# Kernel tuning notes

Hardware: AMD Instinct MI355X
Metric: run time of the kernel (lower is better)

## Reference

```python
import jax, jax.numpy as jnp
import numpy as np


def setup_inputs() -> dict:
    key = jax.random.key(0)
    ks = jax.random.split(key, 12)
    N, E, D_IN, D_H, R, B, G, C, D_E = 50000, 600000, 128, 128, 8, 4, 64, 16, 16
    x = jax.random.normal(ks[0], (N, D_IN), dtype=jnp.float32)
    edge_index = jax.random.randint(ks[1], (2, E), 0, N, dtype=jnp.int64)
    edge_type = jax.random.randint(ks[2], (E,), 0, R, dtype=jnp.int64)
    edge_attr = jax.random.normal(ks[3], (E, D_E), dtype=jnp.float32)
    batch = jnp.sort(jax.random.randint(ks[4], (N,), 0, G, dtype=jnp.int64))
    # RGCNConv basis-decomposition params + root + bias
    basis = jax.random.normal(ks[5], (B, D_IN, D_H), dtype=jnp.float32) / np.sqrt(D_IN)
    comp = jax.random.normal(ks[6], (R, B), dtype=jnp.float32) / np.sqrt(B)
    root = jax.random.normal(ks[7], (D_IN, D_H), dtype=jnp.float32) / np.sqrt(D_IN)
    bias = jnp.zeros((D_H,), dtype=jnp.float32)
    fc_w = jax.random.normal(ks[8], (D_H, C), dtype=jnp.float32) / np.sqrt(D_H)
    fc_b = jnp.zeros((C,), dtype=jnp.float32)
    return {"x": x, "edge_index": edge_index, "edge_type": edge_type,
            "edge_attr": edge_attr, "batch": batch, "num_graphs": 64,
            "basis": basis, "comp": comp, "root": root, "bias": bias,
            "fc_w": fc_w, "fc_b": fc_b}


def reference(x, edge_index, edge_type, edge_attr, batch, num_graphs,
              basis, comp, root, bias, fc_w, fc_b):
    N = x.shape[0]
    R = comp.shape[0]
    src, dst = edge_index[0], edge_index[1]
    # relation weights from basis decomposition: [R, in, out]
    W = jnp.einsum('rb,bio->rio', comp, basis)
    x_src = x[src]  # gather source features [E, in]
    agg = jnp.zeros((N, W.shape[2]), dtype=x.dtype)
    # per-relation mean aggregation (PyG RGCNConv default), summed over relations
    for r in range(R):
        mask = (edge_type == r).astype(x.dtype)  # [E]
        msg = (x_src @ W[r]) * mask[:, None]     # [E, out]
        summed = jax.ops.segment_sum(msg, dst, num_segments=N)
        cnt = jax.ops.segment_sum(mask, dst, num_segments=N)
        agg = agg + summed / jnp.maximum(cnt, 1.0)[:, None]
    h = jax.nn.relu(x @ root + bias + agg)       # [N, hidden]
    # global mean pool over graphs
    pooled_sum = jax.ops.segment_sum(h, batch, num_segments=num_graphs)
    gcnt = jax.ops.segment_sum(jnp.ones((N,), dtype=x.dtype), batch, num_segments=num_graphs)
    pooled = pooled_sum / jnp.maximum(gcnt, 1.0)[:, None]  # [G, hidden]
    return pooled @ fc_w + fc_b                  # [G, num_classes]
```

## Files before the change

kernel.cpp:

```cpp
#include <hip/hip_runtime.h>

static inline int ceil_div(int a, int b){ return (a+b-1)/b; }
static inline size_t align_up(size_t x, size_t a){ return (x + a - 1) / a * a; }

typedef __bf16 bf16x8 __attribute__((ext_vector_type(8)));
typedef float  f32x4  __attribute__((ext_vector_type(4)));

static __device__ inline unsigned short f2bf(float f){
    unsigned int u = __float_as_uint(f);
    unsigned int lsb = (u >> 16) & 1u;
    u += 0x7FFFu + lsb;
    return (unsigned short)(u >> 16);
}
static __device__ inline float bf2f(unsigned short b){
    return __uint_as_float(((unsigned int)b) << 16);
}
static __device__ inline unsigned int packbf(float a, float b){
    return (unsigned int)f2bf(a) | ((unsigned int)f2bf(b) << 16);
}

static __device__ inline void gload_lds16(const void* g, void* l) {
    __builtin_amdgcn_global_load_lds(
        (const __attribute__((address_space(1))) unsigned int*)g,
        (__attribute__((address_space(3))) unsigned int*)l, 16, 0, 0);
}

__global__ void compute_Bt_kernel(const float* __restrict__ comp, const float* __restrict__ basis,
                                  const float* __restrict__ root, unsigned short* __restrict__ Bt,
                                  int B) {
    int idx = blockIdx.x*blockDim.x + threadIdx.x;
    if (idx >= 128*1152) return;
    int o = idx / 1152, kk = idx - o*1152;
    float val;
    if (kk < 1024) {
        int r = kk >> 7, i = kk & 127;
        val = 0.f;
        for (int b = 0; b < B; ++b)
            val += comp[r*B+b] * basis[((size_t)b*128 + i)*128 + o];
    } else {
        val = root[(size_t)(kk-1024)*128 + o];
    }
    Bt[idx] = f2bf(val);
}

__global__ void count_kernel(const int* __restrict__ dst, const int* __restrict__ et,
                             int* __restrict__ cnt, int E, int R) {
    int e = blockIdx.x*blockDim.x + threadIdx.x;
    if (e >= E) return;
    atomicAdd(&cnt[(size_t)dst[e]*R + et[e]], 1);
}

__global__ __launch_bounds__(256)
void scan_block_kernel(const int* __restrict__ in, int* __restrict__ out,
                       int* __restrict__ bsums, int n) {
    __shared__ int tsum[256];
    int t = threadIdx.x;
    int idx0 = blockIdx.x*1024 + t*4;
    int v0 = (idx0+0 < n) ? in[idx0+0] : 0;
    int v1 = (idx0+1 < n) ? in[idx0+1] : 0;
    int v2 = (idx0+2 < n) ? in[idx0+2] : 0;
    int v3 = (idx0+3 < n) ? in[idx0+3] : 0;
    int s = v0+v1+v2+v3;
    tsum[t] = s; __syncthreads();
    for (int off = 1; off < 256; off <<= 1) {
        int x = (t >= off) ? tsum[t-off] : 0;
        __syncthreads();
        tsum[t] += x;
        __syncthreads();
    }
    int run = tsum[t] - s;
    if (idx0+0 < n) out[idx0+0] = run; run += v0;
    if (idx0+1 < n) out[idx0+1] = run; run += v1;
    if (idx0+2 < n) out[idx0+2] = run; run += v2;
    if (idx0+3 < n) out[idx0+3] = run;
    if (bsums && t == 255) bsums[blockIdx.x] = tsum[255];
}

__global__ void scan_add_kernel(int* __restrict__ out, const int* __restrict__ bs,
                                int n, int total) {
    int i = blockIdx.x*blockDim.x + threadIdx.x;
    if (i < n) out[i] += bs[i >> 10];
    if (i == 0) out[n] = total;
}

__global__ void fill_kernel(const int* __restrict__ src, const int* __restrict__ dst,
                            const int* __restrict__ et, int* __restrict__ offsets,
                            int* __restrict__ slot_src, int E, int R) {
    int e = blockIdx.x*blockDim.x + threadIdx.x;
    if (e >= E) return;
    if (e < 4) slot_src[E + e] = 0;
    int bin = dst[e]*R + et[e];
    int slot = atomicAdd(&offsets[bin], 1);
    slot_src[slot] = src[e];
}

__global__ __launch_bounds__(256)
void xb_kernel(const float* __restrict__ x, unsigned int* __restrict__ Xb2, int N) {
    int t = blockIdx.x*blockDim.x + threadIdx.x;
    int n = t >> 6;
    if (n >= N) return;
    int l = t & 63;
    float2 v = reinterpret_cast<const float2*>(x + (size_t)n*128)[l];
    Xb2[(size_t)n*64 + l] = packbf(v.x, v.y);
}

__global__ __launch_bounds__(256)
void aggregate_kernel(const int* __restrict__ offsets, const int* __restrict__ slot_src,
                      const unsigned int* __restrict__ Xb2, unsigned int* __restrict__ Mc2,
                      int N) {
    int gw = (int)((blockIdx.x*blockDim.x + threadIdx.x) >> 6);
    int node = gw >> 2, part = gw & 3;
    if (node >= N) return;
    int l = threadIdx.x & 63;
    int base = node*8 + part*2;
    int lo   = (base == 0) ? 0 : offsets[base-1];
    int bmid = offsets[base];
    int hi   = offsets[base+1];

    float ax0=0.f, ay0=0.f, ax1=0.f, ay1=0.f;

#define ACC2(E_, U_) { \
    float vx_ = bf2f((unsigned short)((U_) & 0xFFFFu)); \
    float vy_ = bf2f((unsigned short)((U_) >> 16)); \
    if ((E_) < bmid) { ax0 += vx_; ay0 += vy_; } \
    else             { ax1 += vx_; ay1 += vy_; } }

    for (int e = lo; e < hi; e += 4) {
        int s0 = slot_src[e];
        int s1 = slot_src[e+1];
        int s2 = slot_src[e+2];
        int s3 = slot_src[e+3];
        unsigned int u0 = Xb2[(size_t)s0*64 + l];
        unsigned int u1 = Xb2[(size_t)s1*64 + l];
        unsigned int u2 = Xb2[(size_t)s2*64 + l];
        unsigned int u3 = Xb2[(size_t)s3*64 + l];
        if (e+1 >= hi) u1 = 0u;
        if (e+2 >= hi) u2 = 0u;
        if (e+3 >= hi) u3 = 0u;
        ACC2(e+0, u0) ACC2(e+1, u1) ACC2(e+2, u2) ACC2(e+3, u3)
    }
#undef ACC2

    unsigned int* Mrow = Mc2 + (size_t)node*512;
    float i0 = 1.f/fmaxf((float)(bmid-lo), 1.f);
    float i1 = 1.f/fmaxf((float)(hi-bmid), 1.f);
    __builtin_nontemporal_store(packbf(ax0*i0, ay0*i0), &Mrow[(2*part+0)*64 + l]);
    __builtin_nontemporal_store(packbf(ax1*i1, ay1*i1), &Mrow[(2*part+1)*64 + l]);
}

__global__ __launch_bounds__(256)
void mfma_gemm_kernel(const unsigned short* __restrict__ Mc,
                      const unsigned short* __restrict__ Xb,
                      const unsigned short* __restrict__ Btc,
                      const float* __restrict__ bias,
                      unsigned short* __restrict__ h, int MBrows) {
    __shared__ char ldsA[64*128];
    __shared__ char ldsB[64*128];

    int tid  = threadIdx.x;
    int lane = tid & 63;
    int wid  = tid >> 6;
    int rg = wid & 1, cg = wid >> 1;
    int fr = lane & 15, kb = lane >> 4;

    int blk = blockIdx.x;
    int q = blk >> 4, rem = blk & 15, c = rem >> 3, m = rem & 7;
    int rb = q*8 + m;
    if (rb >= MBrows) return;
    long m0 = (long)rb * 64;
    int colbase = c * 64;

    int lrow8 = lane >> 3;
    int lcb   = (lane & 7) * 16;

    f32x4 acc[2][2];
    #pragma unroll
    for (int mf = 0; mf < 2; ++mf)
        #pragma unroll
        for (int nf = 0; nf < 2; ++nf) acc[mf][nf] = f32x4{0.f,0.f,0.f,0.f};

    const char* McB = (const char*)Mc;
    const char* XbB = (const char*)Xb;
    const char* BtB = (const char*)Btc;

    for (int t = 0; t < 18; ++t) {
        #pragma unroll
        for (int i = 0; i < 2; ++i) {
            int row = wid*16 + i*8 + lrow8;
            int sw  = lcb ^ ((row & 7) << 4);
            const char* g = (t < 16)
                ? McB + (size_t)(m0 + row)*2048 + t*128 + sw
                : XbB + (size_t)(m0 + row)*256 + (t-16)*128 + sw;
            gload_lds16(g, &ldsA[wid*2048 + i*1024 + lane*16]);
        }
        #pragma unroll
        for (int i = 0; i < 2; ++i) {
            int col = wid*16 + i*8 + lrow8;
            int sw  = lcb ^ ((col & 7) << 4);
            const char* g = BtB + (size_t)(colbase + col)*2304 + t*128 + sw;
            gload_lds16(g, &ldsB[wid*2048 + i*1024 + lane*16]);
        }
        __syncthreads();

        bf16x8 af[2][2], bfr[2][2];
        #pragma unroll
        for (int mf = 0; mf < 2; ++mf) {
            int row = rg*32 + mf*16 + fr;
            #pragma unroll
            for (int kk = 0; kk < 2; ++kk) {
                int byte = row*128 + ((kk*64 + kb*16) ^ ((row & 7) << 4));
                af[mf][kk] = *reinterpret_cast<const bf16x8*>(&ldsA[byte]);
            }
        }
        #pragma unroll
        for (int nf = 0; nf < 2; ++nf) {
            int col = cg*32 + nf*16 + fr;
            #pragma unroll
            for (int kk = 0; kk < 2; ++kk) {
                int byte = col*128 + ((kk*64 + kb*16) ^ ((col & 7) << 4));
                bfr[nf][kk] = *reinterpret_cast<const bf16x8*>(&ldsB[byte]);
            }
        }
        #pragma unroll
        for (int kk = 0; kk < 2; ++kk)
            #pragma unroll
            for (int mf = 0; mf < 2; ++mf)
                #pragma unroll
                for (int nf = 0; nf < 2; ++nf)
                    acc[mf][nf] = __builtin_amdgcn_mfma_f32_16x16x32_bf16(
                        af[mf][kk], bfr[nf][kk], acc[mf][nf], 0, 0, 0);
        __syncthreads();
    }

    float bb[2];
    #pragma unroll
    for (int nf = 0; nf < 2; ++nf) bb[nf] = bias[colbase + cg*32 + nf*16 + fr];

    #pragma unroll
    for (int mf = 0; mf < 2; ++mf)
        #pragma unroll
        for (int q2 = 0; q2 < 4; ++q2) {
            long r = m0 + rg*32 + mf*16 + kb*4 + q2;
            unsigned short* hr = h + (size_t)r*128 + colbase + cg*32;
            #pragma unroll
            for (int nf = 0; nf < 2; ++nf)
                hr[nf*16 + fr] = f2bf(fmaxf(acc[mf][nf][q2] + bb[nf], 0.f));
        }
}

__global__ __launch_bounds__(256)
void pool_kernel(const unsigned int* __restrict__ h2, const int* __restrict__ batch,
                 float* __restrict__ psum, int N) {
    int g = blockIdx.x;
    int t = threadIdx.x;
    int lo = 0, hi = N;
    while (lo < hi) { int mid = (lo+hi) >> 1; if (batch[mid] < g) lo = mid+1; else hi = mid; }
    int s0 = lo;
    hi = N;
    while (lo < hi) { int mid = (lo+hi) >> 1; if (batch[mid] < g+1) lo = mid+1; else hi = mid; }
    int s1 = lo;
    int len = s1 - s0;
    int chunk = blockIdx.y, NC = gridDim.y;
    int a = s0 + (int)((long long)len * chunk / NC);
    int b = s0 + (int)((long long)len * (chunk+1) / NC);

    int d2 = t & 63;
    float ax = 0.f, ay = 0.f;
    for (int row = a + (t >> 6); row < b; row += 4) {
        unsigned int u = h2[(size_t)row*64 + d2];
        ax += bf2f((unsigned short)(u & 0xFFFFu));
        ay += bf2f((unsigned short)(u >> 16));
    }
    atomicAdd(&psum[(size_t)g*128 + 2*d2    ], ax);
    atomicAdd(&psum[(size_t)g*128 + 2*d2 + 1], ay);
}

__global__ void fc_kernel(const float* __restrict__ psum, const int* __restrict__ batch,
                          const float* __restrict__ fw, const float* __restrict__ fb,
                          float* __restrict__ out, int N, int G, int C) {
    int idx = blockIdx.x*blockDim.x + threadIdx.x;
    if (idx >= G*C) return;
    int g = idx / C, cc = idx - g*C;
    int lo = 0, hi = N;
    while (lo < hi) { int mid = (lo+hi) >> 1; if (batch[mid] < g) lo = mid+1; else hi = mid; }
    int s0 = lo;
    hi = N;
    while (lo < hi) { int mid = (lo+hi) >> 1; if (batch[mid] < g+1) lo = mid+1; else hi = mid; }
    float inv = 1.f / fmaxf((float)(lo - s0), 1.f);
    float s = fb[cc];
    #pragma unroll 4
    for (int k = 0; k < 128; ++k)
        s += psum[(size_t)g*128 + k] * inv * fw[(size_t)k*C + cc];
    out[idx] = s;
}

extern "C" void kernel_launch(void* const* d_in, const int* in_sizes, int n_in,
                              void* d_out, int out_size, void* d_ws, size_t ws_size,
                              hipStream_t stream) {
    const float* x       = (const float*)d_in[0];
    const int*   eindex  = (const int*)  d_in[1];
    const int*   etype   = (const int*)  d_in[2];
    const int*   batch   = (const int*)  d_in[4];
    const float* basis   = (const float*)d_in[6];
    const float* comp    = (const float*)d_in[7];
    const float* root    = (const float*)d_in[8];
    const float* bias    = (const float*)d_in[9];
    const float* fc_w    = (const float*)d_in[10];
    const float* fc_b    = (const float*)d_in[11];

    int N  = in_sizes[4];
    int E  = in_sizes[2];
    int C  = in_sizes[11];
    int G  = out_size / C;
    int IO = in_sizes[8];
    int B  = in_sizes[6] / IO;
    int R  = in_sizes[7] / B;
    int NR = N * R;
    int MB = ceil_div(N, 64);
    int Mpad = MB * 64;
    int grid_gemm = ceil_div(MB, 8) * 16;

    const int* src = eindex;
    const int* dst = eindex + E;

    char* base = (char*)d_ws;
    size_t off = 0;
    auto alloc = [&](size_t bytes) -> char* {
        char* p = base + off;
        off = align_up(off + bytes, 256);
        return p;
    };
    unsigned short* Bt  = (unsigned short*)alloc(sizeof(unsigned short)*128*1152);
    int*   cnt      = (int*)  alloc(sizeof(int)*(size_t)NR);
    float* psum     = (float*)alloc(sizeof(float)*(size_t)G*128);
    int*   offsets  = (int*)  alloc(sizeof(int)*((size_t)NR+1));
    int*   bsums    = (int*)  alloc(sizeof(int)*1024);
    int*   slot_src = (int*)  alloc(sizeof(int)*((size_t)E+4));
    unsigned short* h  = (unsigned short*)alloc(sizeof(unsigned short)*(size_t)Mpad*128);
    unsigned short* Xb = (unsigned short*)alloc(sizeof(unsigned short)*(size_t)Mpad*128);
    unsigned short* Mc = (unsigned short*)alloc(sizeof(unsigned short)*(size_t)Mpad*1024);

    hipMemsetAsync(cnt, 0, (size_t)((char*)(psum + (size_t)G*128) - (char*)cnt), stream);
    compute_Bt_kernel<<<ceil_div(128*1152,256),256,0,stream>>>(comp, basis, root, Bt, B);
    count_kernel<<<ceil_div(E,256),256,0,stream>>>(dst, etype, cnt, E, R);

    int nb = ceil_div(NR, 1024);
    scan_block_kernel<<<nb,256,0,stream>>>(cnt, offsets, bsums, NR);
    scan_block_kernel<<<1,256,0,stream>>>(bsums, bsums, nullptr, nb);
    scan_add_kernel<<<ceil_div(NR,256),256,0,stream>>>(offsets, bsums, NR, E);

    fill_kernel<<<ceil_div(E,256),256,0,stream>>>(src, dst, etype, offsets, slot_src, E, R);

    xb_kernel<<<ceil_div(N*64,256),256,0,stream>>>(x, (unsigned int*)Xb, N);
    aggregate_kernel<<<ceil_div(N*4*64,256),256,0,stream>>>(offsets, slot_src,
                                                            (const unsigned int*)Xb,
                                                            (unsigned int*)Mc, N);

    mfma_gemm_kernel<<<grid_gemm,256,0,stream>>>(Mc, Xb, Bt, bias, h, MB);

    pool_kernel<<<dim3(G,8),256,0,stream>>>((const unsigned int*)h, batch, psum, N);
    fc_kernel<<<ceil_div(G*C,256),256,0,stream>>>(psum, batch, fc_w, fc_b,
                                                  (float*)d_out, N, G, C);
}
```

Measured before the change: 217.4 us.

## Widen GEMM tile to full output width with double-buffered LDS staging

The GEMM block now computes all 128 output columns for its 64 rows instead of splitting into two column halves. This halves re-reads of the large aggregated-message matrix. LDS tiles are double-buffered so the next k-slice load is issued before computing the current one. The fill kernel also stores pre-shifted row offsets so the aggregate gather skips a 64-bit multiply. The trade-off is more LDS and accumulator registers per block, with half as many blocks.

```diff
diff --git a/kernel.cpp b/kernel.cpp
--- a/kernel.cpp
+++ b/kernel.cpp
@@ -85,13 +85,13 @@
 
 __global__ void fill_kernel(const int* __restrict__ src, const int* __restrict__ dst,
                             const int* __restrict__ et, int* __restrict__ offsets,
-                            int* __restrict__ slot_src, int E, int R) {
+                            int* __restrict__ slot_off, int E, int R) {
     int e = blockIdx.x*blockDim.x + threadIdx.x;
     if (e >= E) return;
-    if (e < 4) slot_src[E + e] = 0;
+    if (e < 4) slot_off[E + e] = 0;
     int bin = dst[e]*R + et[e];
     int slot = atomicAdd(&offsets[bin], 1);
-    slot_src[slot] = src[e];
+    slot_off[slot] = src[e] << 6;
 }
 
 __global__ __launch_bounds__(256)
@@ -105,7 +105,7 @@
 }
 
 __global__ __launch_bounds__(256)
-void aggregate_kernel(const int* __restrict__ offsets, const int* __restrict__ slot_src,
+void aggregate_kernel(const int* __restrict__ offsets, const int* __restrict__ slot_off,
                       const unsigned int* __restrict__ Xb2, unsigned int* __restrict__ Mc2,
                       int N) {
     int gw = (int)((blockIdx.x*blockDim.x + threadIdx.x) >> 6);
@@ -126,14 +126,14 @@
     else             { ax1 += vx_; ay1 += vy_; } }
 
     for (int e = lo; e < hi; e += 4) {
-        int s0 = slot_src[e];
-        int s1 = slot_src[e+1];
-        int s2 = slot_src[e+2];
-        int s3 = slot_src[e+3];
-        unsigned int u0 = Xb2[(size_t)s0*64 + l];
-        unsigned int u1 = Xb2[(size_t)s1*64 + l];
-        unsigned int u2 = Xb2[(size_t)s2*64 + l];
-        unsigned int u3 = Xb2[(size_t)s3*64 + l];
+        int s0 = slot_off[e];
+        int s1 = slot_off[e+1];
+        int s2 = slot_off[e+2];
+        int s3 = slot_off[e+3];
+        unsigned int u0 = Xb2[(unsigned)(s0 + l)];
+        unsigned int u1 = Xb2[(unsigned)(s1 + l)];
+        unsigned int u2 = Xb2[(unsigned)(s2 + l)];
+        unsigned int u3 = Xb2[(unsigned)(s3 + l)];
         if (e+1 >= hi) u1 = 0u;
         if (e+2 >= hi) u2 = 0u;
         if (e+3 >= hi) u3 = 0u;
@@ -153,37 +153,31 @@
                       const unsigned short* __restrict__ Xb,
                       const unsigned short* __restrict__ Btc,
                       const float* __restrict__ bias,
-                      unsigned short* __restrict__ h, int MBrows) {
-    __shared__ char ldsA[64*128];
-    __shared__ char ldsB[64*128];
+                      unsigned short* __restrict__ h) {
+    __shared__ char ldsA[2][64*128];
+    __shared__ char ldsB[2][128*128];
 
     int tid  = threadIdx.x;
     int lane = tid & 63;
     int wid  = tid >> 6;
     int rg = wid & 1, cg = wid >> 1;
     int fr = lane & 15, kb = lane >> 4;
-
-    int blk = blockIdx.x;
-    int q = blk >> 4, rem = blk & 15, c = rem >> 3, m = rem & 7;
-    int rb = q*8 + m;
-    if (rb >= MBrows) return;
-    long m0 = (long)rb * 64;
-    int colbase = c * 64;
+    long m0 = (long)blockIdx.x * 64;
 
     int lrow8 = lane >> 3;
     int lcb   = (lane & 7) * 16;
-
-    f32x4 acc[2][2];
-    #pragma unroll
-    for (int mf = 0; mf < 2; ++mf)
-        #pragma unroll
-        for (int nf = 0; nf < 2; ++nf) acc[mf][nf] = f32x4{0.f,0.f,0.f,0.f};
 
     const char* McB = (const char*)Mc;
     const char* XbB = (const char*)Xb;
     const char* BtB = (const char*)Btc;
 
-    for (int t = 0; t < 18; ++t) {
+    f32x4 acc[2][4];
+    #pragma unroll
+    for (int mf = 0; mf < 2; ++mf)
+        #pragma unroll
+        for (int nf = 0; nf < 4; ++nf) acc[mf][nf] = f32x4{0.f,0.f,0.f,0.f};
+
+    auto stage = [&](int t, int buf) {
         #pragma unroll
         for (int i = 0; i < 2; ++i) {
             int row = wid*16 + i*8 + lrow8;
@@ -191,34 +185,41 @@
             const char* g = (t < 16)
                 ? McB + (size_t)(m0 + row)*2048 + t*128 + sw
                 : XbB + (size_t)(m0 + row)*256 + (t-16)*128 + sw;
-            gload_lds16(g, &ldsA[wid*2048 + i*1024 + lane*16]);
-        }
-        #pragma unroll
-        for (int i = 0; i < 2; ++i) {
-            int col = wid*16 + i*8 + lrow8;
+            gload_lds16(g, &ldsA[buf][wid*2048 + i*1024 + lane*16]);
+        }
+        #pragma unroll
+        for (int i = 0; i < 4; ++i) {
+            int col = wid*32 + i*8 + lrow8;
             int sw  = lcb ^ ((col & 7) << 4);
-            const char* g = BtB + (size_t)(colbase + col)*2304 + t*128 + sw;
-            gload_lds16(g, &ldsB[wid*2048 + i*1024 + lane*16]);
-        }
-        __syncthreads();
-
-        bf16x8 af[2][2], bfr[2][2];
+            const char* g = BtB + (size_t)col*2304 + t*128 + sw;
+            gload_lds16(g, &ldsB[buf][wid*4096 + i*1024 + lane*16]);
+        }
+    };
+
+    stage(0, 0);
+    __syncthreads();
+
+    for (int t = 0; t < 18; ++t) {
+        int cur = t & 1;
+        if (t + 1 < 18) stage(t + 1, cur ^ 1);
+
+        bf16x8 af[2][2], bfr[4][2];
         #pragma unroll
         for (int mf = 0; mf < 2; ++mf) {
             int row = rg*32 + mf*16 + fr;
             #pragma unroll
             for (int kk = 0; kk < 2; ++kk) {
                 int byte = row*128 + ((kk*64 + kb*16) ^ ((row & 7) << 4));
-                af[mf][kk] = *reinterpret_cast<const bf16x8*>(&ldsA[byte]);
+                af[mf][kk] = *reinterpret_cast<const bf16x8*>(&ldsA[cur][byte]);
             }
         }
         #pragma unroll
-        for (int nf = 0; nf < 2; ++nf) {
-            int col = cg*32 + nf*16 + fr;
+        for (int nf = 0; nf < 4; ++nf) {
+            int col = cg*64 + nf*16 + fr;
             #pragma unroll
             for (int kk = 0; kk < 2; ++kk) {
                 int byte = col*128 + ((kk*64 + kb*16) ^ ((col & 7) << 4));
-                bfr[nf][kk] = *reinterpret_cast<const bf16x8*>(&ldsB[byte]);
+                bfr[nf][kk] = *reinterpret_cast<const bf16x8*>(&ldsB[cur][byte]);
             }
         }
         #pragma unroll
@@ -226,25 +227,25 @@
             #pragma unroll
             for (int mf = 0; mf < 2; ++mf)
                 #pragma unroll
-                for (int nf = 0; nf < 2; ++nf)
+                for (int nf = 0; nf < 4; ++nf)
                     acc[mf][nf] = __builtin_amdgcn_mfma_f32_16x16x32_bf16(
                         af[mf][kk], bfr[nf][kk], acc[mf][nf], 0, 0, 0);
         __syncthreads();
     }
 
-    float bb[2];
+    float bb[4];
     #pragma unroll
-    for (int nf = 0; nf < 2; ++nf) bb[nf] = bias[colbase + cg*32 + nf*16 + fr];
+    for (int nf = 0; nf < 4; ++nf) bb[nf] = bias[cg*64 + nf*16 + fr];
 
     #pragma unroll
     for (int mf = 0; mf < 2; ++mf)
         #pragma unroll
-        for (int q2 = 0; q2 < 4; ++q2) {
-            long r = m0 + rg*32 + mf*16 + kb*4 + q2;
-            unsigned short* hr = h + (size_t)r*128 + colbase + cg*32;
+        for (int q = 0; q < 4; ++q) {
+            long r = m0 + rg*32 + mf*16 + kb*4 + q;
+            unsigned short* hr = h + (size_t)r*128 + cg*64;
             #pragma unroll
-            for (int nf = 0; nf < 2; ++nf)
-                hr[nf*16 + fr] = f2bf(fmaxf(acc[mf][nf][q2] + bb[nf], 0.f));
+            for (int nf = 0; nf < 4; ++nf)
+                hr[nf*16 + fr] = f2bf(fmaxf(acc[mf][nf][q] + bb[nf], 0.f));
         }
 }
 
@@ -318,7 +319,6 @@
     int NR = N * R;
     int MB = ceil_div(N, 64);
     int Mpad = MB * 64;
-    int grid_gemm = ceil_div(MB, 8) * 16;
 
     const int* src = eindex;
     const int* dst = eindex + E;
@@ -335,7 +335,7 @@
     float* psum     = (float*)alloc(sizeof(float)*(size_t)G*128);
     int*   offsets  = (int*)  alloc(sizeof(int)*((size_t)NR+1));
     int*   bsums    = (int*)  alloc(sizeof(int)*1024);
-    int*   slot_src = (int*)  alloc(sizeof(int)*((size_t)E+4));
+    int*   slot_off = (int*)  alloc(sizeof(int)*((size_t)E+4));
     unsigned short* h  = (unsigned short*)alloc(sizeof(unsigned short)*(size_t)Mpad*128);
     unsigned short* Xb = (unsigned short*)alloc(sizeof(unsigned short)*(size_t)Mpad*128);
     unsigned short* Mc = (unsigned short*)alloc(sizeof(unsigned short)*(size_t)Mpad*1024);
@@ -349,14 +349,14 @@
     scan_block_kernel<<<1,256,0,stream>>>(bsums, bsums, nullptr, nb);
     scan_add_kernel<<<ceil_div(NR,256),256,0,stream>>>(offsets, bsums, NR, E);
 
-    fill_kernel<<<ceil_div(E,256),256,0,stream>>>(src, dst, etype, offsets, slot_src, E, R);
+    fill_kernel<<<ceil_div(E,256),256,0,stream>>>(src, dst, etype, offsets, slot_off, E, R);
 
     xb_kernel<<<ceil_div(N*64,256),256,0,stream>>>(x, (unsigned int*)Xb, N);
-    aggregate_kernel<<<ceil_div(N*4*64,256),256,0,stream>>>(offsets, slot_src,
+    aggregate_kernel<<<ceil_div(N*4*64,256),256,0,stream>>>(offsets, slot_off,
                                                             (const unsigned int*)Xb,
                                                             (unsigned int*)Mc, N);
 
-    mfma_gemm_kernel<<<grid_gemm,256,0,stream>>>(Mc, Xb, Bt, bias, h, MB);
+    mfma_gemm_kernel<<<MB,256,0,stream>>>(Mc, Xb, Bt, bias, h);
 
     pool_kernel<<<dim3(G,8),256,0,stream>>>((const unsigned int*)h, batch, psum, N);
     fc_kernel<<<ceil_div(G*C,256),256,0,stream>>>(psum, batch, fc_w, fc_b,
```

Result: slower. 224.2 us (+3.1%).

## Fuse preprocessing kernels, precompute scaled gather offsets, fuse pool with FC

Applied to the files above, without the earlier changes.

Merges the memset, basis-weight build and bf16 conversion of x into one grid-stride kernel, removing a memset and a launch. Fill now stores src<<6 so the aggregate gather uses a 32-bit add instead of a 64-bit multiply. Pooling and the final FC are fused into one 512-thread block per graph that reduces in shared memory, dropping global atomics and one launch. The trade-off is that pooling now runs on only G blocks instead of G×8, so it has less parallelism.

```diff
diff --git a/kernel.cpp b/kernel.cpp
--- a/kernel.cpp
+++ b/kernel.cpp
@@ -25,22 +25,32 @@
         (__attribute__((address_space(3))) unsigned int*)l, 16, 0, 0);
 }
 
-__global__ void compute_Bt_kernel(const float* __restrict__ comp, const float* __restrict__ basis,
-                                  const float* __restrict__ root, unsigned short* __restrict__ Bt,
-                                  int B) {
-    int idx = blockIdx.x*blockDim.x + threadIdx.x;
-    if (idx >= 128*1152) return;
-    int o = idx / 1152, kk = idx - o*1152;
-    float val;
-    if (kk < 1024) {
-        int r = kk >> 7, i = kk & 127;
-        val = 0.f;
-        for (int b = 0; b < B; ++b)
-            val += comp[r*B+b] * basis[((size_t)b*128 + i)*128 + o];
-    } else {
-        val = root[(size_t)(kk-1024)*128 + o];
-    }
-    Bt[idx] = f2bf(val);
+__global__ __launch_bounds__(256)
+void pre_kernel(const float* __restrict__ comp, const float* __restrict__ basis,
+                const float* __restrict__ root, unsigned short* __restrict__ Bt, int B,
+                const float* __restrict__ x, unsigned int* __restrict__ Xb2, int N,
+                int* __restrict__ cnt, int NR) {
+    int gtid = blockIdx.x*blockDim.x + threadIdx.x;
+    int gsz  = gridDim.x*blockDim.x;
+    for (int i = gtid; i < NR; i += gsz) cnt[i] = 0;
+    for (int idx = gtid; idx < 128*1152; idx += gsz) {
+        int o = idx / 1152, kk = idx - o*1152;
+        float val;
+        if (kk < 1024) {
+            int r = kk >> 7, i = kk & 127;
+            val = 0.f;
+            for (int b = 0; b < B; ++b)
+                val += comp[r*B+b] * basis[((size_t)b*128 + i)*128 + o];
+        } else {
+            val = root[(size_t)(kk-1024)*128 + o];
+        }
+        Bt[idx] = f2bf(val);
+    }
+    for (int tt = gtid; tt < N*64; tt += gsz) {
+        int n = tt >> 6, l = tt & 63;
+        float2 v = reinterpret_cast<const float2*>(x + (size_t)n*128)[l];
+        Xb2[(size_t)n*64 + l] = packbf(v.x, v.y);
+    }
 }
 
 __global__ void count_kernel(const int* __restrict__ dst, const int* __restrict__ et,
@@ -85,27 +95,17 @@
 
 __global__ void fill_kernel(const int* __restrict__ src, const int* __restrict__ dst,
                             const int* __restrict__ et, int* __restrict__ offsets,
-                            int* __restrict__ slot_src, int E, int R) {
+                            int* __restrict__ slot_off, int E, int R) {
     int e = blockIdx.x*blockDim.x + threadIdx.x;
     if (e >= E) return;
-    if (e < 4) slot_src[E + e] = 0;
+    if (e < 4) slot_off[E + e] = 0;
     int bin = dst[e]*R + et[e];
     int slot = atomicAdd(&offsets[bin], 1);
-    slot_src[slot] = src[e];
+    slot_off[slot] = src[e] << 6;
 }
 
 __global__ __launch_bounds__(256)
-void xb_kernel(const float* __restrict__ x, unsigned int* __restrict__ Xb2, int N) {
-    int t = blockIdx.x*blockDim.x + threadIdx.x;
-    int n = t >> 6;
-    if (n >= N) return;
-    int l = t & 63;
-    float2 v = reinterpret_cast<const float2*>(x + (size_t)n*128)[l];
-    Xb2[(size_t)n*64 + l] = packbf(v.x, v.y);
-}
-
-__global__ __launch_bounds__(256)
-void aggregate_kernel(const int* __restrict__ offsets, const int* __restrict__ slot_src,
+void aggregate_kernel(const int* __restrict__ offsets, const int* __restrict__ slot_off,
                       const unsigned int* __restrict__ Xb2, unsigned int* __restrict__ Mc2,
                       int N) {
     int gw = (int)((blockIdx.x*blockDim.x + threadIdx.x) >> 6);
@@ -126,14 +126,14 @@
     else             { ax1 += vx_; ay1 += vy_; } }
 
     for (int e = lo; e < hi; e += 4) {
-        int s0 = slot_src[e];
-        int s1 = slot_src[e+1];
-        int s2 = slot_src[e+2];
-        int s3 = slot_src[e+3];
-        unsigned int u0 = Xb2[(size_t)s0*64 + l];
-        unsigned int u1 = Xb2[(size_t)s1*64 + l];
-        unsigned int u2 = Xb2[(size_t)s2*64 + l];
-        unsigned int u3 = Xb2[(size_t)s3*64 + l];
+        int s0 = slot_off[e];
+        int s1 = slot_off[e+1];
+        int s2 = slot_off[e+2];
+        int s3 = slot_off[e+3];
+        unsigned int u0 = Xb2[(unsigned)(s0 + l)];
+        unsigned int u1 = Xb2[(unsigned)(s1 + l)];
+        unsigned int u2 = Xb2[(unsigned)(s2 + l)];
+        unsigned int u3 = Xb2[(unsigned)(s3 + l)];
         if (e+1 >= hi) u1 = 0u;
         if (e+2 >= hi) u2 = 0u;
         if (e+3 >= hi) u3 = 0u;
@@ -248,9 +248,10 @@
         }
 }
 
-__global__ __launch_bounds__(256)
-void pool_kernel(const unsigned int* __restrict__ h2, const int* __restrict__ batch,
-                 float* __restrict__ psum, int N) {
+__global__ __launch_bounds__(512)
+void pool_fc_kernel(const unsigned int* __restrict__ h2, const int* __restrict__ batch,
+                    const float* __restrict__ fw, const float* __restrict__ fb,
+                    float* __restrict__ out, int N, int C) {
     int g = blockIdx.x;
     int t = threadIdx.x;
     int lo = 0, hi = N;
@@ -259,39 +260,27 @@
     hi = N;
     while (lo < hi) { int mid = (lo+hi) >> 1; if (batch[mid] < g+1) lo = mid+1; else hi = mid; }
     int s1 = lo;
-    int len = s1 - s0;
-    int chunk = blockIdx.y, NC = gridDim.y;
-    int a = s0 + (int)((long long)len * chunk / NC);
-    int b = s0 + (int)((long long)len * (chunk+1) / NC);
 
     int d2 = t & 63;
     float ax = 0.f, ay = 0.f;
-    for (int row = a + (t >> 6); row < b; row += 4) {
+    for (int row = s0 + (t >> 6); row < s1; row += 8) {
         unsigned int u = h2[(size_t)row*64 + d2];
         ax += bf2f((unsigned short)(u & 0xFFFFu));
         ay += bf2f((unsigned short)(u >> 16));
     }
-    atomicAdd(&psum[(size_t)g*128 + 2*d2    ], ax);
-    atomicAdd(&psum[(size_t)g*128 + 2*d2 + 1], ay);
-}
-
-__global__ void fc_kernel(const float* __restrict__ psum, const int* __restrict__ batch,
-                          const float* __restrict__ fw, const float* __restrict__ fb,
-                          float* __restrict__ out, int N, int G, int C) {
-    int idx = blockIdx.x*blockDim.x + threadIdx.x;
-    if (idx >= G*C) return;
-    int g = idx / C, cc = idx - g*C;
-    int lo = 0, hi = N;
-    while (lo < hi) { int mid = (lo+hi) >> 1; if (batch[mid] < g) lo = mid+1; else hi = mid; }
-    int s0 = lo;
-    hi = N;
-    while (lo < hi) { int mid = (lo+hi) >> 1; if (batch[mid] < g+1) lo = mid+1; else hi = mid; }
-    float inv = 1.f / fmaxf((float)(lo - s0), 1.f);
-    float s = fb[cc];
-    #pragma unroll 4
-    for (int k = 0; k < 128; ++k)
-        s += psum[(size_t)g*128 + k] * inv * fw[(size_t)k*C + cc];
-    out[idx] = s;
+    __shared__ float ps[128];
+    if (t < 128) ps[t] = 0.f;
+    __syncthreads();
+    atomicAdd(&ps[2*d2],   ax);
+    atomicAdd(&ps[2*d2+1], ay);
+    __syncthreads();
+    if (t < C) {
+        float inv = 1.f / fmaxf((float)(s1 - s0), 1.f);
+        float s = 0.f;
+        #pragma unroll 4
+        for (int k = 0; k < 128; ++k) s += ps[k] * fw[(size_t)k*C + t];
+        out[(size_t)g*C + t] = s * inv + fb[t];
+    }
 }
 
 extern "C" void kernel_launch(void* const* d_in, const int* in_sizes, int n_in,
@@ -332,16 +321,15 @@
     };
     unsigned short* Bt  = (unsigned short*)alloc(sizeof(unsigned short)*128*1152);
     int*   cnt      = (int*)  alloc(sizeof(int)*(size_t)NR);
-    float* psum     = (float*)alloc(sizeof(float)*(size_t)G*128);
     int*   offsets  = (int*)  alloc(sizeof(int)*((size_t)NR+1));
     int*   bsums    = (int*)  alloc(sizeof(int)*1024);
-    int*   slot_src = (int*)  alloc(sizeof(int)*((size_t)E+4));
+    int*   slot_off = (int*)  alloc(sizeof(int)*((size_t)E+4));
     unsigned short* h  = (unsigned short*)alloc(sizeof(unsigned short)*(size_t)Mpad*128);
     unsigned short* Xb = (unsigned short*)alloc(sizeof(unsigned short)*(size_t)Mpad*128);
     unsigned short* Mc = (unsigned short*)alloc(sizeof(unsigned short)*(size_t)Mpad*1024);
 
-    hipMemsetAsync(cnt, 0, (size_t)((char*)(psum + (size_t)G*128) - (char*)cnt), stream);
-    compute_Bt_kernel<<<ceil_div(128*1152,256),256,0,stream>>>(comp, basis, root, Bt, B);
+    pre_kernel<<<1024,256,0,stream>>>(comp, basis, root, Bt, B,
+                                      x, (unsigned int*)Xb, N, cnt, NR);
     count_kernel<<<ceil_div(E,256),256,0,stream>>>(dst, etype, cnt, E, R);
 
     int nb = ceil_div(NR, 1024);
@@ -349,16 +337,14 @@
     scan_block_kernel<<<1,256,0,stream>>>(bsums, bsums, nullptr, nb);
     scan_add_kernel<<<ceil_div(NR,256),256,0,stream>>>(offsets, bsums, NR, E);
 
-    fill_kernel<<<ceil_div(E,256),256,0,stream>>>(src, dst, etype, offsets, slot_src, E, R);
-
-    xb_kernel<<<ceil_div(N*64,256),256,0,stream>>>(x, (unsigned int*)Xb, N);
-    aggregate_kernel<<<ceil_div(N*4*64,256),256,0,stream>>>(offsets, slot_src,
+    fill_kernel<<<ceil_div(E,256),256,0,stream>>>(src, dst, etype, offsets, slot_off, E, R);
+
+    aggregate_kernel<<<ceil_div(N*4*64,256),256,0,stream>>>(offsets, slot_off,
                                                             (const unsigned int*)Xb,
                                                             (unsigned int*)Mc, N);
 
     mfma_gemm_kernel<<<grid_gemm,256,0,stream>>>(Mc, Xb, Bt, bias, h, MB);
 
-    pool_kernel<<<dim3(G,8),256,0,stream>>>((const unsigned int*)h, batch, psum, N);
-    fc_kernel<<<ceil_div(G*C,256),256,0,stream>>>(psum, batch, fc_w, fc_b,
-                                                  (float*)d_out, N, G, C);
-}
+    pool_fc_kernel<<<G,512,0,stream>>>((const unsigned int*)h, batch, fc_w, fc_b,
+                                       (float*)d_out, N, C);
+}
```

Measured after the change: 213.5 us. Within noise of the previous version (-1.8%).
